# Optimization experiments

Measured on AMD Instinct MI355X. Metric: run time of the kernel, lower is better.

Reference implementation:

```python
import jax, jax.numpy as jnp
import numpy as np

EPS = 1e-5
K = 20


def knn_idx(x, k):
    # x: (B, N, C) -> (B, N, k) indices of k nearest neighbors (incl. self)
    x2 = jnp.sum(x * x, axis=-1)                         # (B, N)
    inner = jnp.einsum('bnc,bmc->bnm', x, x)             # (B, N, N)
    neg_dist = 2.0 * inner - x2[:, :, None] - x2[:, None, :]
    _, idx = jax.lax.top_k(neg_dist, k)                  # (B, N, k)
    return idx


def graph_feature(x, idx):
    # x: (B, N, C), idx: (B, N, k) -> (B, N, k, 2C) = cat([x_j - x_i, x_i])
    nbr = jax.vmap(lambda xb, ib: xb[ib])(x, idx)        # (B, N, k, C)
    xi = jnp.broadcast_to(x[:, :, None, :], nbr.shape)
    return jnp.concatenate([nbr - xi, xi], axis=-1)


def bn_lrelu(x, gamma, beta):
    # eval-mode BatchNorm (running_mean=0, running_var=1) + LeakyReLU(0.2)
    y = x * (gamma / jnp.sqrt(1.0 + EPS)) + beta
    return jnp.where(y >= 0, y, 0.2 * y)


def edge_conv(x, W, gamma, beta, k):
    # x: (B, N, C) -> (B, N, O); 1x1 conv over edge features + max over k
    idx = knn_idx(x, k)
    feat = graph_feature(x, idx)                         # (B, N, k, 2C)
    y = jnp.einsum('bnkc,oc->bnko', feat, W)
    y = bn_lrelu(y, gamma, beta)
    return jnp.max(y, axis=2)                            # (B, N, O)


def setup_inputs() -> dict:
    key = jax.random.key(0)
    ks = jax.random.split(key, 7)
    d = {
        'points': jax.random.normal(ks[0], (8, 2048, 3), dtype=jnp.float32),
        'W1': jax.random.normal(ks[1], (64, 6), dtype=jnp.float32) * 0.1,
        'W2': jax.random.normal(ks[2], (64, 128), dtype=jnp.float32) * 0.1,
        'W3': jax.random.normal(ks[3], (128, 128), dtype=jnp.float32) * 0.1,
        'W4': jax.random.normal(ks[4], (256, 256), dtype=jnp.float32) * 0.1,
        'W5': jax.random.normal(ks[5], (1024, 512), dtype=jnp.float32) * 0.1,
    }
    for name, c in [('1', 64), ('2', 64), ('3', 128), ('4', 256), ('5', 1024)]:
        d['g' + name] = jnp.ones((c,), dtype=jnp.float32)
        d['b' + name] = jnp.zeros((c,), dtype=jnp.float32)
    return d


def reference(points, W1, W2, W3, W4, W5, g1, g2, g3, g4, g5, b1, b2, b3, b4, b5):
    x1 = edge_conv(points, W1, g1, b1, K)                # (B, N, 64)
    x2 = edge_conv(x1, W2, g2, b2, K)                    # (B, N, 64)
    x3 = edge_conv(x2, W3, g3, b3, K)                    # (B, N, 128)
    x4 = edge_conv(x3, W4, g4, b4, K)                    # (B, N, 256)
    x_cat = jnp.concatenate([x1, x2, x3, x4], axis=-1)   # (B, N, 512)
    feat = bn_lrelu(jnp.einsum('bnc,oc->bno', x_cat, W5), g5, b5)  # (B, N, 1024)
    max_pool = jnp.max(feat, axis=1)
    avg_pool = jnp.mean(feat, axis=1)
    return jnp.concatenate([max_pool, avg_pool], axis=-1)  # (B, 2048)
```

## Files before the change

kernel.cpp:

```cpp
#include <hip/hip_runtime.h>
#include <math.h>

#define BATCH 8
#define NPTS 2048
#define KNN 20
#define BN_TOTAL (BATCH * NPTS)
#define EPSV 1e-5f

typedef __attribute__((ext_vector_type(8))) short short8v;
typedef __attribute__((ext_vector_type(4))) float floatx4;

__global__ __launch_bounds__(256) void x2_kernel(const float* __restrict__ x, int C, int ldx,
                                                 float* __restrict__ x2) {
    int i = blockIdx.x * 256 + threadIdx.x;
    if (i >= BN_TOTAL) return;
    const float* xr = x + (size_t)i * ldx;
    float s = 0.f;
    if ((ldx & 3) == 0 && (C & 3) == 0) {
        const float4* xr4 = (const float4*)xr;
        for (int c = 0; c < (C >> 2); ++c) {
            float4 v = xr4[c];
            s = fmaf(v.x, v.x, s); s = fmaf(v.y, v.y, s);
            s = fmaf(v.z, v.z, s); s = fmaf(v.w, v.w, s);
        }
    } else {
        for (int c = 0; c < C; ++c) s = fmaf(xr[c], xr[c], s);
    }
    x2[i] = s;
}

__global__ __launch_bounds__(256) void dist_kernel(const float* __restrict__ x,
                                                   const float* __restrict__ x2,
                                                   int C, int ldx, int b0,
                                                   float* __restrict__ S) {
    __shared__ float As[16][132];
    __shared__ float Bs[16][132];
    int z = blockIdx.z;
    int b = b0 + z;
    int i0 = blockIdx.x * 128, j0 = blockIdx.y * 128;
    const float* xb = x + (size_t)b * NPTS * ldx;
    int tid = threadIdx.x;
    int tm = tid >> 4, tn = tid & 15;

    float acc[8][8] = {};
    int KT = (C + 15) >> 4;
    for (int kt = 0; kt < KT; ++kt) {
        int k0 = kt << 4;
#pragma unroll
        for (int s = tid; s < 512; s += 256) {
            int r = s >> 2, c4 = s & 3;
            int kk = k0 + c4 * 4;
            float va[4], vb[4];
            if (kk + 3 < C && (ldx & 3) == 0) {
                float4 a = *(const float4*)&xb[(size_t)(i0 + r) * ldx + kk];
                float4 bv = *(const float4*)&xb[(size_t)(j0 + r) * ldx + kk];
                va[0] = a.x; va[1] = a.y; va[2] = a.z; va[3] = a.w;
                vb[0] = bv.x; vb[1] = bv.y; vb[2] = bv.z; vb[3] = bv.w;
            } else {
#pragma unroll
                for (int u = 0; u < 4; ++u) {
                    int k = kk + u;
                    va[u] = (k < C) ? xb[(size_t)(i0 + r) * ldx + k] : 0.f;
                    vb[u] = (k < C) ? xb[(size_t)(j0 + r) * ldx + k] : 0.f;
                }
            }
#pragma unroll
            for (int u = 0; u < 4; ++u) {
                As[c4 * 4 + u][r] = va[u];
                Bs[c4 * 4 + u][r] = vb[u];
            }
        }
        __syncthreads();
#pragma unroll
        for (int k = 0; k < 16; ++k) {
            float4 a0 = *(const float4*)&As[k][tm * 8];
            float4 a1 = *(const float4*)&As[k][tm * 8 + 4];
            float4 c0 = *(const float4*)&Bs[k][tn * 8];
            float4 c1 = *(const float4*)&Bs[k][tn * 8 + 4];
            float av[8] = {a0.x, a0.y, a0.z, a0.w, a1.x, a1.y, a1.z, a1.w};
            float bv[8] = {c0.x, c0.y, c0.z, c0.w, c1.x, c1.y, c1.z, c1.w};
#pragma unroll
            for (int mi = 0; mi < 8; ++mi)
#pragma unroll
                for (int ni = 0; ni < 8; ++ni)
                    acc[mi][ni] = fmaf(av[mi], bv[ni], acc[mi][ni]);
        }
        __syncthreads();
    }

    const float* x2b = x2 + (size_t)b * NPTS;
    float xj[8];
#pragma unroll
    for (int u = 0; u < 8; ++u) xj[u] = x2b[j0 + tn * 8 + u];
#pragma unroll
    for (int mi = 0; mi < 8; ++mi) {
        float xi = x2b[i0 + tm * 8 + mi];
        float4 o0, o1;
        o0.x = 2.f * acc[mi][0] - xi - xj[0];
        o0.y = 2.f * acc[mi][1] - xi - xj[1];
        o0.z = 2.f * acc[mi][2] - xi - xj[2];
        o0.w = 2.f * acc[mi][3] - xi - xj[3];
        o1.x = 2.f * acc[mi][4] - xi - xj[4];
        o1.y = 2.f * acc[mi][5] - xi - xj[5];
        o1.z = 2.f * acc[mi][6] - xi - xj[6];
        o1.w = 2.f * acc[mi][7] - xi - xj[7];
        size_t rowp = ((size_t)z * NPTS + i0 + tm * 8 + mi) * NPTS + j0 + tn * 8;
        *(float4*)&S[rowp] = o0;
        *(float4*)&S[rowp + 4] = o1;
    }
}

__global__ __launch_bounds__(256) void topk_kernel(const float* __restrict__ S, int b0,
                                                   int* __restrict__ idx_out) {
    int lane = threadIdx.x & 63, w = threadIdx.x >> 6;
    int row = blockIdx.x * 4 + w;
    const float4* S4 = (const float4*)(S + (size_t)row * NPTS);

    float v[32];
    float lm = -INFINITY; int li = 0;
#pragma unroll
    for (int r4 = 0; r4 < 8; ++r4) {
        float4 f = S4[lane * 8 + r4];
        v[r4 * 4 + 0] = f.x; v[r4 * 4 + 1] = f.y;
        v[r4 * 4 + 2] = f.z; v[r4 * 4 + 3] = f.w;
    }
#pragma unroll
    for (int q = 0; q < 32; ++q)
        if (v[q] > lm) { lm = v[q]; li = q; }

    int sel = 0;
    for (int it = 0; it < KNN; ++it) {
        float bv = lm;
        int bi = (lane << 5) | li;
#pragma unroll
        for (int d = 1; d < 64; d <<= 1) {
            float ov = __shfl_xor(bv, d);
            int oi = __shfl_xor(bi, d);
            if (ov > bv || (ov == bv && oi < bi)) { bv = ov; bi = oi; }
        }
        if (lane == it) sel = bi;
        if ((bi >> 5) == lane) {
            int r = bi & 31;
#pragma unroll
            for (int q = 0; q < 32; ++q)
                if (q == r) v[q] = -INFINITY;
            lm = -INFINITY; li = 0;
#pragma unroll
            for (int q = 0; q < 32; ++q)
                if (v[q] > lm) { lm = v[q]; li = q; }
        }
    }
    int z = row >> 11, i = row & 2047;
    int bn = (b0 + z) * NPTS + i;
    if (lane < KNN) idx_out[bn * KNN + lane] = sel;
}

__global__ __launch_bounds__(256) void pq_gemm(const float* __restrict__ X, int C, int ldx,
                                               const float* __restrict__ W, int O,
                                               float* __restrict__ PQ) {
    __shared__ float As[32][68];
    __shared__ float Bs[32][68];
    int i0 = blockIdx.x * 64, j0 = blockIdx.y * 64;
    int tid = threadIdx.x;
    int tm = tid >> 4, tn = tid & 15;
    int N2 = 2 * O;

    float acc[4][4] = {};
    int KT = (C + 31) >> 5;
    for (int kt = 0; kt < KT; ++kt) {
        int k0 = kt << 5;
        for (int e = tid; e < 2048; e += 256) {
            int m = e >> 5, k = e & 31;
            int kk = k0 + k;
            As[k][m] = (kk < C) ? X[(size_t)(i0 + m) * ldx + kk] : 0.f;
            int o = j0 + m;
            float wv = 0.f;
            if (kk < C)
                wv = (o < O) ? W[(size_t)o * 2 * C + kk] : W[(size_t)(o - O) * 2 * C + C + kk];
            Bs[k][m] = wv;
        }
        __syncthreads();
#pragma unroll
        for (int k = 0; k < 32; ++k) {
            float4 a = *(const float4*)&As[k][tm * 4];
            float4 bb = *(const float4*)&Bs[k][tn * 4];
            float av[4] = {a.x, a.y, a.z, a.w};
            float bv[4] = {bb.x, bb.y, bb.z, bb.w};
#pragma unroll
            for (int mi = 0; mi < 4; ++mi)
#pragma unroll
                for (int ni = 0; ni < 4; ++ni)
                    acc[mi][ni] = fmaf(av[mi], bv[ni], acc[mi][ni]);
        }
        __syncthreads();
    }
#pragma unroll
    for (int mi = 0; mi < 4; ++mi) {
        float4 o;
        o.x = acc[mi][0]; o.y = acc[mi][1]; o.z = acc[mi][2]; o.w = acc[mi][3];
        *(float4*)&PQ[(size_t)(i0 + tm * 4 + mi) * N2 + j0 + tn * 4] = o;
    }
}

__global__ __launch_bounds__(256) void gmax_kernel(const float* __restrict__ PQ,
                                                   const int* __restrict__ idx, int O, int oshift,
                                                   const float* __restrict__ gamma,
                                                   const float* __restrict__ beta,
                                                   float* __restrict__ out, int ldo) {
    __shared__ int s_idx[4][KNN];
    int rpb = 256 >> oshift;
    int lr = threadIdx.x >> oshift;
    int o = threadIdx.x & (O - 1);
    int bn = blockIdx.x * rpb + lr;
    int b = bn >> 11;
    if (o < KNN) s_idx[lr][o] = idx[bn * KNN + o];
    __syncthreads();
    const float inv = 1.0f / sqrtf(1.0f + EPSV);
    int N2 = 2 * O;
    size_t brow = (size_t)(b << 11);
    float mx = -INFINITY, mn = INFINITY;
#pragma unroll
    for (int k = 0; k < KNN; ++k) {
        float v = PQ[(brow + s_idx[lr][k]) * N2 + o];
        mx = fmaxf(mx, v);
        mn = fminf(mn, v);
    }
    float pn = PQ[(size_t)bn * N2 + o];
    float qn = PQ[(size_t)bn * N2 + O + o];
    float sc = gamma[o] * inv;
    float m = (sc >= 0.f) ? mx : mn;
    float z = sc * (m - pn + qn) + beta[o];
    out[(size_t)bn * ldo + o] = (z >= 0.f) ? z : 0.2f * z;
}

__device__ __forceinline__ unsigned short bf16_rne(float x) {
    union { float f; unsigned u; } cv; cv.f = x;
    unsigned r = (cv.u + 0x7fffu + ((cv.u >> 16) & 1u)) >> 16;
    return (unsigned short)r;
}
__global__ __launch_bounds__(256) void split_bf16_kernel(const float* __restrict__ in, int n4,
                                                         unsigned short* __restrict__ hi,
                                                         unsigned short* __restrict__ lo) {
    int i = blockIdx.x * 256 + threadIdx.x;
    if (i >= n4) return;
    float4 v = ((const float4*)in)[i];
    float vv[4] = {v.x, v.y, v.z, v.w};
    ushort4 h, l;
    unsigned short hh[4], ll[4];
#pragma unroll
    for (int u = 0; u < 4; ++u) {
        unsigned short hb = bf16_rne(vv[u]);
        union { unsigned u32; float f; } hf; hf.u32 = ((unsigned)hb) << 16;
        hh[u] = hb;
        ll[u] = bf16_rne(vv[u] - hf.f);
    }
    h.x = hh[0]; h.y = hh[1]; h.z = hh[2]; h.w = hh[3];
    l.x = ll[0]; l.y = ll[1]; l.z = ll[2]; l.w = ll[3];
    *(ushort4*)(hi + (size_t)i * 4) = h;
    *(ushort4*)(lo + (size_t)i * 4) = l;
}

__global__ __launch_bounds__(256) void final_mfma(const unsigned short* __restrict__ Xhi,
                                                  const unsigned short* __restrict__ Xlo,
                                                  const unsigned short* __restrict__ Whi,
                                                  const unsigned short* __restrict__ Wlo,
                                                  const float* __restrict__ g5,
                                                  const float* __restrict__ b5,
                                                  float* __restrict__ part) {
    __shared__ __align__(16) char As[128 * 64];
    __shared__ __align__(16) char Bs[128 * 64];
    __shared__ float sredM[2][128];
    __shared__ float sredS[2][128];

    int tid = threadIdx.x;
    int i0 = blockIdx.x * 128;
    int j0 = blockIdx.y * 128;
    int lane = tid & 63, w = tid >> 6;
    int wr = w >> 1, wc = w & 1;

    int rowA = tid >> 2, q = tid & 3;
    auto swz = [](int row, int qq) { return (row * 64 + qq * 16) ^ ((row & 7) << 4); };
    int wa0 = swz(rowA, q), wa1 = swz(rowA + 64, q);

    int fr = lane & 15, slot = lane >> 4;
    int aoff[4], boff[4];
#pragma unroll
    for (int m = 0; m < 4; ++m) {
        int ra = wr * 64 + m * 16 + fr;
        aoff[m] = (ra * 64 + slot * 16) ^ ((ra & 7) << 4);
        int rb = wc * 64 + m * 16 + fr;
        boff[m] = (rb * 64 + slot * 16) ^ ((rb & 7) << 4);
    }

    floatx4 acc[4][4];
#pragma unroll
    for (int m = 0; m < 4; ++m)
#pragma unroll
        for (int n = 0; n < 4; ++n)
            acc[m][n] = (floatx4){0.f, 0.f, 0.f, 0.f};

    uint4 ra0, ra1, rb0, rb1;
    auto prefetch = [&](int it) {
        int seg = it >> 4;
        int kk = (it & 15) * 32;
        const unsigned short* Ab = ((seg < 2) ? Xhi : Xlo) + (size_t)i0 * 512 + kk + q * 8;
        const unsigned short* Bb = ((seg == 1) ? Wlo : Whi) + (size_t)j0 * 512 + kk + q * 8;
        ra0 = *(const uint4*)(Ab + (size_t)rowA * 512);
        ra1 = *(const uint4*)(Ab + (size_t)(rowA + 64) * 512);
        rb0 = *(const uint4*)(Bb + (size_t)rowA * 512);
        rb1 = *(const uint4*)(Bb + (size_t)(rowA + 64) * 512);
    };

    prefetch(0);
    for (int it = 0; it < 48; ++it) {
        __syncthreads();
        *(uint4*)(As + wa0) = ra0;
        *(uint4*)(As + wa1) = ra1;
        *(uint4*)(Bs + wa0) = rb0;
        *(uint4*)(Bs + wa1) = rb1;
        __syncthreads();
        if (it < 47) prefetch(it + 1);
        short8v af[4], bf[4];
#pragma unroll
        for (int m = 0; m < 4; ++m) af[m] = *(const short8v*)(As + aoff[m]);
#pragma unroll
        for (int n = 0; n < 4; ++n) bf[n] = *(const short8v*)(Bs + boff[n]);
#pragma unroll
        for (int m = 0; m < 4; ++m)
#pragma unroll
            for (int n = 0; n < 4; ++n)
                acc[m][n] = __builtin_amdgcn_mfma_f32_16x16x32_bf16(af[m], bf[n], acc[m][n], 0, 0, 0);
    }

    const float inv = 1.0f / sqrtf(1.0f + EPSV);
#pragma unroll
    for (int n = 0; n < 4; ++n) {
        int o = j0 + wc * 64 + n * 16 + fr;
        float sc = g5[o] * inv;
        float bi = b5[o];
        float mx = -INFINITY, sm = 0.f;
#pragma unroll
        for (int m = 0; m < 4; ++m)
#pragma unroll
            for (int r = 0; r < 4; ++r) {
                float z = fmaf(sc, acc[m][n][r], bi);
                z = (z >= 0.f) ? z : 0.2f * z;
                mx = fmaxf(mx, z);
                sm += z;
            }
#pragma unroll
        for (int d = 16; d < 64; d <<= 1) {
            mx = fmaxf(mx, __shfl_xor(mx, d));
            sm += __shfl_xor(sm, d);
        }
        if (slot == 0) {
            sredM[wr][wc * 64 + n * 16 + fr] = mx;
            sredS[wr][wc * 64 + n * 16 + fr] = sm;
        }
    }
    __syncthreads();
    if (tid < 128) {
        float m = fmaxf(sredM[0][tid], sredM[1][tid]);
        float s = sredS[0][tid] + sredS[1][tid];
        int b = i0 >> 11, nt = (i0 >> 7) & 15;
        size_t base = (size_t)((b * 16 + nt) * 2) * 1024 + j0 + tid;
        part[base] = m;
        part[base + 1024] = s;
    }
}

__global__ __launch_bounds__(256) void freduce_kernel(const float* __restrict__ part,
                                                      float* __restrict__ out) {
    int t = blockIdx.x * 256 + threadIdx.x;
    if (t >= 8 * 1024) return;
    int b = t >> 10, o = t & 1023;
    float m = -INFINITY, s = 0.f;
#pragma unroll
    for (int nt = 0; nt < 16; ++nt) {
        size_t base = (size_t)((b * 16 + nt) * 2) * 1024 + o;
        m = fmaxf(m, part[base]);
        s += part[base + 1024];
    }
    out[b * 2048 + o] = m;
    out[b * 2048 + 1024 + o] = s * (1.0f / 2048.0f);
}

extern "C" void kernel_launch(void* const* d_in, const int* in_sizes, int n_in,
                              void* d_out, int out_size, void* d_ws, size_t ws_size,
                              hipStream_t stream) {
    const float* points = (const float*)d_in[0];
    const float* W1 = (const float*)d_in[1];
    const float* W2 = (const float*)d_in[2];
    const float* W3 = (const float*)d_in[3];
    const float* W4 = (const float*)d_in[4];
    const float* W5 = (const float*)d_in[5];
    const float* g1 = (const float*)d_in[6];
    const float* b1 = (const float*)d_in[7];
    const float* g2 = (const float*)d_in[8];
    const float* b2 = (const float*)d_in[9];
    const float* g3 = (const float*)d_in[10];
    const float* b3 = (const float*)d_in[11];
    const float* g4 = (const float*)d_in[12];
    const float* b4 = (const float*)d_in[13];
    const float* g5 = (const float*)d_in[14];
    const float* b5 = (const float*)d_in[15];
    float* out = (float*)d_out;

    const size_t f_xcat = (size_t)BN_TOTAL * 512;
    const size_t f_w5 = (size_t)1024 * 512;
    const size_t f_x2 = BN_TOTAL;
    const size_t f_idx = (size_t)BN_TOTAL * KNN;
    const size_t f_part = (size_t)8 * 16 * 2 * 1024;
    const size_t f_bf16 = f_xcat + f_w5;
    const size_t fixedf = f_xcat + f_x2 + f_idx + f_part + f_bf16;
    auto needB = [&](int c) {
        size_t spq = (size_t)c * NPTS * NPTS;
        if (spq < f_xcat) spq = f_xcat;
        return 4ull * (fixedf + spq);
    };
    int cB = 2;
    if (ws_size >= needB(8)) cB = 8;
    else if (ws_size >= needB(4)) cB = 4;
    size_t spq_f = (size_t)cB * NPTS * NPTS;
    if (spq_f < f_xcat) spq_f = f_xcat;

    float* xcat = (float*)d_ws;
    float* SPQ = xcat + f_xcat;
    float* x2 = SPQ + spq_f;
    int* idx = (int*)(x2 + f_x2);
    float* part = (float*)(idx + f_idx);
    unsigned short* Xhi = (unsigned short*)(part + f_part);
    unsigned short* Xlo = Xhi + f_xcat;
    unsigned short* Whi = Xlo + f_xcat;
    unsigned short* Wlo = Whi + f_w5;

    auto layer = [&](const float* xin, int C, int ldx, const float* W, int O, int oshift,
                     const float* ga, const float* be, float* xout) {
        x2_kernel<<<(BN_TOTAL + 255) / 256, 256, 0, stream>>>(xin, C, ldx, x2);
        for (int b0 = 0; b0 < BATCH; b0 += cB) {
            dist_kernel<<<dim3(16, 16, cB), 256, 0, stream>>>(xin, x2, C, ldx, b0, SPQ);
            topk_kernel<<<cB * 512, 256, 0, stream>>>(SPQ, b0, idx);
        }
        pq_gemm<<<dim3(BN_TOTAL / 64, (2 * O) / 64), 256, 0, stream>>>(xin, C, ldx, W, O, SPQ);
        int rpb = 256 >> oshift;
        gmax_kernel<<<BN_TOTAL / rpb, 256, 0, stream>>>(SPQ, idx, O, oshift, ga, be, xout, 512);
    };

    layer(points,     3,   3,   W1, 64,  6, g1, b1, xcat + 0);
    layer(xcat + 0,   64,  512, W2, 64,  6, g2, b2, xcat + 64);
    layer(xcat + 64,  64,  512, W3, 128, 7, g3, b3, xcat + 128);
    layer(xcat + 128, 128, 512, W4, 256, 8, g4, b4, xcat + 256);

    split_bf16_kernel<<<(int)((f_xcat / 4 + 255) / 256), 256, 0, stream>>>(xcat, (int)(f_xcat / 4), Xhi, Xlo);
    split_bf16_kernel<<<(int)((f_w5 / 4 + 255) / 256), 256, 0, stream>>>(W5, (int)(f_w5 / 4), Whi, Wlo);
    final_mfma<<<dim3(BN_TOTAL / 128, 1024 / 128), 256, 0, stream>>>(Xhi, Xlo, Whi, Wlo, g5, b5, part);
    freduce_kernel<<<(8 * 1024 + 255) / 256, 256, 0, stream>>>(part, out);
}
```

Baseline: 966.1 us.

## Fuse distance GEMM and top-k selection into one streaming KNN kernel

Replaces the separate distance-matrix kernel (which wrote a full per-batch NxN score matrix to global memory) and the top-k kernel with a single templated kernel. Each block owns 64 query rows, streams over 128-column candidate tiles and keeps a running top-20 list per row in shared memory, using ballot and shuffle reductions to insert only candidates that beat the current minimum. This removes the large global write and read of the score matrix and the batch-chunk launch loop. In exchange the grid is small (256 blocks), insertion work is serialized per row, and the host code specializes launches per layer.

```diff
diff --git a/kernel.cpp b/kernel.cpp
--- a/kernel.cpp
+++ b/kernel.cpp
@@ -29,130 +29,137 @@
     x2[i] = s;
 }
 
-__global__ __launch_bounds__(256) void dist_kernel(const float* __restrict__ x,
-                                                   const float* __restrict__ x2,
-                                                   int C, int ldx, int b0,
-                                                   float* __restrict__ S) {
-    __shared__ float As[16][132];
-    __shared__ float Bs[16][132];
-    int z = blockIdx.z;
-    int b = b0 + z;
-    int i0 = blockIdx.x * 128, j0 = blockIdx.y * 128;
-    const float* xb = x + (size_t)b * NPTS * ldx;
+template <int C, int LDX>
+__global__ __launch_bounds__(512) void knn_fused(const float* __restrict__ x,
+                                                 const float* __restrict__ x2,
+                                                 int* __restrict__ idx_out) {
+    constexpr int BK = (C >= 32) ? 32 : C;
+    constexpr int KT = (C + BK - 1) / BK;
+    __shared__ float As[C][68];
+    __shared__ float Bs[BK][132];
+    __shared__ float tv[64][20];
+    __shared__ int   ti[64][20];
+
     int tid = threadIdx.x;
-    int tm = tid >> 4, tn = tid & 15;
-
-    float acc[8][8] = {};
-    int KT = (C + 15) >> 4;
-    for (int kt = 0; kt < KT; ++kt) {
-        int k0 = kt << 4;
-#pragma unroll
-        for (int s = tid; s < 512; s += 256) {
-            int r = s >> 2, c4 = s & 3;
-            int kk = k0 + c4 * 4;
-            float va[4], vb[4];
-            if (kk + 3 < C && (ldx & 3) == 0) {
-                float4 a = *(const float4*)&xb[(size_t)(i0 + r) * ldx + kk];
-                float4 bv = *(const float4*)&xb[(size_t)(j0 + r) * ldx + kk];
-                va[0] = a.x; va[1] = a.y; va[2] = a.z; va[3] = a.w;
-                vb[0] = bv.x; vb[1] = bv.y; vb[2] = bv.z; vb[3] = bv.w;
+    int b = blockIdx.y;
+    int i0 = blockIdx.x * 64;
+    int bn0 = (b << 11) + i0;
+    const float* xb = x + (size_t)b * NPTS * LDX;
+    const float* x2b = x2 + (b << 11);
+    int tn = tid & 31;
+    int tm = tid >> 5;
+    int g = (tid >> 5) & 1;
+
+    for (int e = tid; e < 64 * KNN; e += 512) {
+        tv[e / KNN][e % KNN] = -INFINITY;
+        ti[e / KNN][e % KNN] = 0x7fffffff;
+    }
+    if (C == 3) {
+        for (int e = tid; e < 64 * 3; e += 512) {
+            int r = e / 3, k = e % 3;
+            As[k][r] = xb[(size_t)(i0 + r) * LDX + k];
+        }
+    } else {
+        for (int e = tid; e < 64 * (C / 4); e += 512) {
+            int r = e / (C / 4), c4 = e % (C / 4);
+            float4 v = *(const float4*)&xb[(size_t)(i0 + r) * LDX + c4 * 4];
+            As[c4 * 4 + 0][r] = v.x; As[c4 * 4 + 1][r] = v.y;
+            As[c4 * 4 + 2][r] = v.z; As[c4 * 4 + 3][r] = v.w;
+        }
+    }
+    float x2i[4];
+#pragma unroll
+    for (int mi = 0; mi < 4; ++mi) x2i[mi] = x2b[i0 + tm * 4 + mi];
+    __syncthreads();
+
+    for (int jt = 0; jt < 16; ++jt) {
+        int j0 = jt << 7;
+        float acc[4][4];
+#pragma unroll
+        for (int mi = 0; mi < 4; ++mi)
+#pragma unroll
+            for (int ni = 0; ni < 4; ++ni) acc[mi][ni] = 0.f;
+
+        for (int kt = 0; kt < KT; ++kt) {
+            __syncthreads();
+            if (C == 3) {
+                for (int e = tid; e < 128 * 3; e += 512) {
+                    int col = e / 3, k = e % 3;
+                    Bs[k][col] = xb[(size_t)(j0 + col) * LDX + k];
+                }
             } else {
-#pragma unroll
-                for (int u = 0; u < 4; ++u) {
-                    int k = kk + u;
-                    va[u] = (k < C) ? xb[(size_t)(i0 + r) * ldx + k] : 0.f;
-                    vb[u] = (k < C) ? xb[(size_t)(j0 + r) * ldx + k] : 0.f;
+                for (int e = tid; e < 128 * (BK / 4); e += 512) {
+                    int col = e >> 3, c4 = e & 7;
+                    float4 v = *(const float4*)&xb[(size_t)(j0 + col) * LDX + kt * BK + c4 * 4];
+                    Bs[c4 * 4 + 0][col] = v.x; Bs[c4 * 4 + 1][col] = v.y;
+                    Bs[c4 * 4 + 2][col] = v.z; Bs[c4 * 4 + 3][col] = v.w;
                 }
             }
-#pragma unroll
-            for (int u = 0; u < 4; ++u) {
-                As[c4 * 4 + u][r] = va[u];
-                Bs[c4 * 4 + u][r] = vb[u];
+            __syncthreads();
+#pragma unroll
+            for (int k = 0; k < BK; ++k) {
+                float4 a = *(const float4*)&As[kt * BK + k][tm * 4];
+                float2 b0 = *(const float2*)&Bs[k][tn * 4];
+                float2 b1 = *(const float2*)&Bs[k][tn * 4 + 2];
+                float av[4] = {a.x, a.y, a.z, a.w};
+                float bv[4] = {b0.x, b0.y, b1.x, b1.y};
+#pragma unroll
+                for (int mi = 0; mi < 4; ++mi)
+#pragma unroll
+                    for (int ni = 0; ni < 4; ++ni)
+                        acc[mi][ni] = fmaf(av[mi], bv[ni], acc[mi][ni]);
             }
         }
-        __syncthreads();
-#pragma unroll
-        for (int k = 0; k < 16; ++k) {
-            float4 a0 = *(const float4*)&As[k][tm * 8];
-            float4 a1 = *(const float4*)&As[k][tm * 8 + 4];
-            float4 c0 = *(const float4*)&Bs[k][tn * 8];
-            float4 c1 = *(const float4*)&Bs[k][tn * 8 + 4];
-            float av[8] = {a0.x, a0.y, a0.z, a0.w, a1.x, a1.y, a1.z, a1.w};
-            float bv[8] = {c0.x, c0.y, c0.z, c0.w, c1.x, c1.y, c1.z, c1.w};
-#pragma unroll
-            for (int mi = 0; mi < 8; ++mi)
-#pragma unroll
-                for (int ni = 0; ni < 8; ++ni)
-                    acc[mi][ni] = fmaf(av[mi], bv[ni], acc[mi][ni]);
-        }
-        __syncthreads();
-    }
-
-    const float* x2b = x2 + (size_t)b * NPTS;
-    float xj[8];
-#pragma unroll
-    for (int u = 0; u < 8; ++u) xj[u] = x2b[j0 + tn * 8 + u];
-#pragma unroll
-    for (int mi = 0; mi < 8; ++mi) {
-        float xi = x2b[i0 + tm * 8 + mi];
-        float4 o0, o1;
-        o0.x = 2.f * acc[mi][0] - xi - xj[0];
-        o0.y = 2.f * acc[mi][1] - xi - xj[1];
-        o0.z = 2.f * acc[mi][2] - xi - xj[2];
-        o0.w = 2.f * acc[mi][3] - xi - xj[3];
-        o1.x = 2.f * acc[mi][4] - xi - xj[4];
-        o1.y = 2.f * acc[mi][5] - xi - xj[5];
-        o1.z = 2.f * acc[mi][6] - xi - xj[6];
-        o1.w = 2.f * acc[mi][7] - xi - xj[7];
-        size_t rowp = ((size_t)z * NPTS + i0 + tm * 8 + mi) * NPTS + j0 + tn * 8;
-        *(float4*)&S[rowp] = o0;
-        *(float4*)&S[rowp + 4] = o1;
-    }
-}
-
-__global__ __launch_bounds__(256) void topk_kernel(const float* __restrict__ S, int b0,
-                                                   int* __restrict__ idx_out) {
-    int lane = threadIdx.x & 63, w = threadIdx.x >> 6;
-    int row = blockIdx.x * 4 + w;
-    const float4* S4 = (const float4*)(S + (size_t)row * NPTS);
-
-    float v[32];
-    float lm = -INFINITY; int li = 0;
-#pragma unroll
-    for (int r4 = 0; r4 < 8; ++r4) {
-        float4 f = S4[lane * 8 + r4];
-        v[r4 * 4 + 0] = f.x; v[r4 * 4 + 1] = f.y;
-        v[r4 * 4 + 2] = f.z; v[r4 * 4 + 3] = f.w;
-    }
-#pragma unroll
-    for (int q = 0; q < 32; ++q)
-        if (v[q] > lm) { lm = v[q]; li = q; }
-
-    int sel = 0;
-    for (int it = 0; it < KNN; ++it) {
-        float bv = lm;
-        int bi = (lane << 5) | li;
-#pragma unroll
-        for (int d = 1; d < 64; d <<= 1) {
-            float ov = __shfl_xor(bv, d);
-            int oi = __shfl_xor(bi, d);
-            if (ov > bv || (ov == bv && oi < bi)) { bv = ov; bi = oi; }
-        }
-        if (lane == it) sel = bi;
-        if ((bi >> 5) == lane) {
-            int r = bi & 31;
-#pragma unroll
-            for (int q = 0; q < 32; ++q)
-                if (q == r) v[q] = -INFINITY;
-            lm = -INFINITY; li = 0;
-#pragma unroll
-            for (int q = 0; q < 32; ++q)
-                if (v[q] > lm) { lm = v[q]; li = q; }
-        }
-    }
-    int z = row >> 11, i = row & 2047;
-    int bn = (b0 + z) * NPTS + i;
-    if (lane < KNN) idx_out[bn * KNN + lane] = sel;
+
+        float x2j[4];
+#pragma unroll
+        for (int u = 0; u < 4; ++u) x2j[u] = x2b[j0 + tn * 4 + u];
+#pragma unroll
+        for (int mi = 0; mi < 4; ++mi)
+#pragma unroll
+            for (int ni = 0; ni < 4; ++ni)
+                acc[mi][ni] = 2.f * acc[mi][ni] - x2i[mi] - x2j[ni];
+
+#pragma unroll
+        for (int mi = 0; mi < 4; ++mi) {
+            int r = tm * 4 + mi;
+            float lmax = acc[mi][0]; int lidx = j0 + tn * 4;
+#pragma unroll
+            for (int ni = 1; ni < 4; ++ni)
+                if (acc[mi][ni] > lmax) { lmax = acc[mi][ni]; lidx = j0 + tn * 4 + ni; }
+            float vmin = tv[r][KNN - 1];
+            unsigned grp = (unsigned)(__ballot(lmax > vmin) >> (g * 32));
+            while (grp) {
+                float bv = lmax; int bj = lidx;
+#pragma unroll
+                for (int d = 1; d < 32; d <<= 1) {
+                    float ov = __shfl_xor(bv, d);
+                    int oj = __shfl_xor(bj, d);
+                    if (ov > bv || (ov == bv && oj < bj)) { bv = ov; bj = oj; }
+                }
+                int p = KNN - 1;
+                while (p > 0 && tv[r][p - 1] < bv) {
+                    tv[r][p] = tv[r][p - 1]; ti[r][p] = ti[r][p - 1]; --p;
+                }
+                tv[r][p] = bv; ti[r][p] = bj;
+                vmin = tv[r][KNN - 1];
+                if (((bj - j0) >> 2) == tn) {
+                    int nk = bj & 3;
+#pragma unroll
+                    for (int ni = 0; ni < 4; ++ni)
+                        if (ni == nk) acc[mi][ni] = -INFINITY;
+                    lmax = acc[mi][0]; lidx = j0 + tn * 4;
+#pragma unroll
+                    for (int ni = 1; ni < 4; ++ni)
+                        if (acc[mi][ni] > lmax) { lmax = acc[mi][ni]; lidx = j0 + tn * 4 + ni; }
+                }
+                grp = (unsigned)(__ballot(lmax > vmin) >> (g * 32));
+            }
+        }
+    }
+    __syncthreads();
+    for (int e = tid; e < 64 * KNN; e += 512)
+        idx_out[(size_t)(bn0 + e / KNN) * KNN + e % KNN] = ti[e / KNN][e % KNN];
 }
 
 __global__ __launch_bounds__(256) void pq_gemm(const float* __restrict__ X, int C, int ldx,
@@ -411,22 +418,10 @@
     const size_t f_x2 = BN_TOTAL;
     const size_t f_idx = (size_t)BN_TOTAL * KNN;
     const size_t f_part = (size_t)8 * 16 * 2 * 1024;
-    const size_t f_bf16 = f_xcat + f_w5;
-    const size_t fixedf = f_xcat + f_x2 + f_idx + f_part + f_bf16;
-    auto needB = [&](int c) {
-        size_t spq = (size_t)c * NPTS * NPTS;
-        if (spq < f_xcat) spq = f_xcat;
-        return 4ull * (fixedf + spq);
-    };
-    int cB = 2;
-    if (ws_size >= needB(8)) cB = 8;
-    else if (ws_size >= needB(4)) cB = 4;
-    size_t spq_f = (size_t)cB * NPTS * NPTS;
-    if (spq_f < f_xcat) spq_f = f_xcat;
 
     float* xcat = (float*)d_ws;
     float* SPQ = xcat + f_xcat;
-    float* x2 = SPQ + spq_f;
+    float* x2 = SPQ + f_xcat;
     int* idx = (int*)(x2 + f_x2);
     float* part = (float*)(idx + f_idx);
     unsigned short* Xhi = (unsigned short*)(part + f_part);
@@ -434,22 +429,25 @@
     unsigned short* Whi = Xlo + f_xcat;
     unsigned short* Wlo = Whi + f_w5;
 
-    auto layer = [&](const float* xin, int C, int ldx, const float* W, int O, int oshift,
-                     const float* ga, const float* be, float* xout) {
-        x2_kernel<<<(BN_TOTAL + 255) / 256, 256, 0, stream>>>(xin, C, ldx, x2);
-        for (int b0 = 0; b0 < BATCH; b0 += cB) {
-            dist_kernel<<<dim3(16, 16, cB), 256, 0, stream>>>(xin, x2, C, ldx, b0, SPQ);
-            topk_kernel<<<cB * 512, 256, 0, stream>>>(SPQ, b0, idx);
-        }
-        pq_gemm<<<dim3(BN_TOTAL / 64, (2 * O) / 64), 256, 0, stream>>>(xin, C, ldx, W, O, SPQ);
-        int rpb = 256 >> oshift;
-        gmax_kernel<<<BN_TOTAL / rpb, 256, 0, stream>>>(SPQ, idx, O, oshift, ga, be, xout, 512);
-    };
-
-    layer(points,     3,   3,   W1, 64,  6, g1, b1, xcat + 0);
-    layer(xcat + 0,   64,  512, W2, 64,  6, g2, b2, xcat + 64);
-    layer(xcat + 64,  64,  512, W3, 128, 7, g3, b3, xcat + 128);
-    layer(xcat + 128, 128, 512, W4, 256, 8, g4, b4, xcat + 256);
+    x2_kernel<<<64, 256, 0, stream>>>(points, 3, 3, x2);
+    knn_fused<3, 3><<<dim3(32, 8), 512, 0, stream>>>(points, x2, idx);
+    pq_gemm<<<dim3(256, 2), 256, 0, stream>>>(points, 3, 3, W1, 64, SPQ);
+    gmax_kernel<<<BN_TOTAL / 4, 256, 0, stream>>>(SPQ, idx, 64, 6, g1, b1, xcat + 0, 512);
+
+    x2_kernel<<<64, 256, 0, stream>>>(xcat + 0, 64, 512, x2);
+    knn_fused<64, 512><<<dim3(32, 8), 512, 0, stream>>>(xcat + 0, x2, idx);
+    pq_gemm<<<dim3(256, 2), 256, 0, stream>>>(xcat + 0, 64, 512, W2, 64, SPQ);
+    gmax_kernel<<<BN_TOTAL / 4, 256, 0, stream>>>(SPQ, idx, 64, 6, g2, b2, xcat + 64, 512);
+
+    x2_kernel<<<64, 256, 0, stream>>>(xcat + 64, 64, 512, x2);
+    knn_fused<64, 512><<<dim3(32, 8), 512, 0, stream>>>(xcat + 64, x2, idx);
+    pq_gemm<<<dim3(256, 4), 256, 0, stream>>>(xcat + 64, 64, 512, W3, 128, SPQ);
+    gmax_kernel<<<BN_TOTAL / 2, 256, 0, stream>>>(SPQ, idx, 128, 7, g3, b3, xcat + 128, 512);
+
+    x2_kernel<<<64, 256, 0, stream>>>(xcat + 128, 128, 512, x2);
+    knn_fused<128, 512><<<dim3(32, 8), 512, 0, stream>>>(xcat + 128, x2, idx);
+    pq_gemm<<<dim3(256, 8), 256, 0, stream>>>(xcat + 128, 128, 512, W4, 256, SPQ);
+    gmax_kernel<<<BN_TOTAL, 256, 0, stream>>>(SPQ, idx, 256, 8, g4, b4, xcat + 256, 512);
 
     split_bf16_kernel<<<(int)((f_xcat / 4 + 255) / 256), 256, 0, stream>>>(xcat, (int)(f_xcat / 4), Xhi, Xlo);
     split_bf16_kernel<<<(int)((f_w5 / 4 + 255) / 256), 256, 0, stream>>>(W5, (int)(f_w5 / 4), Whi, Wlo);
```

Result: slower. 2.547 ms (+163.7%).

## Fuse distance GEMM with per-tile top-k and merge candidates instead of full matrix

Applied to the files above, without the earlier changes.

The distance kernel now runs a local top-20 selection inside each 128x128 tile via 16-lane shuffles and writes only 20 candidates per row per column tile. A second kernel merges the 320 candidates per row into the final 20 neighbours. This removes writing and re-reading the full N×N distance matrix and the batch-chunking loop, and the workspace is restructured into a shared union buffer. The cost is a serial 20-iteration shuffle loop per row inside the GEMM kernel, which adds register pressure and latency.

```diff
diff --git a/kernel.cpp b/kernel.cpp
--- a/kernel.cpp
+++ b/kernel.cpp
@@ -6,6 +6,7 @@
 #define KNN 20
 #define BN_TOTAL (BATCH * NPTS)
 #define EPSV 1e-5f
+#define NT 16
 
 typedef __attribute__((ext_vector_type(8))) short short8v;
 typedef __attribute__((ext_vector_type(4))) float floatx4;
@@ -29,15 +30,15 @@
     x2[i] = s;
 }
 
-__global__ __launch_bounds__(256) void dist_kernel(const float* __restrict__ x,
+__global__ __launch_bounds__(256) void dtop_kernel(const float* __restrict__ x,
                                                    const float* __restrict__ x2,
-                                                   int C, int ldx, int b0,
-                                                   float* __restrict__ S) {
+                                                   int C, int ldx,
+                                                   float2* __restrict__ cand) {
     __shared__ float As[16][132];
     __shared__ float Bs[16][132];
-    int z = blockIdx.z;
-    int b = b0 + z;
-    int i0 = blockIdx.x * 128, j0 = blockIdx.y * 128;
+    int b = blockIdx.z;
+    int jt = blockIdx.y;
+    int i0 = blockIdx.x * 128, j0 = jt * 128;
     const float* xb = x + (size_t)b * NPTS * ldx;
     int tid = threadIdx.x;
     int tm = tid >> 4, tn = tid & 15;
@@ -95,64 +96,87 @@
 #pragma unroll
     for (int mi = 0; mi < 8; ++mi) {
         float xi = x2b[i0 + tm * 8 + mi];
-        float4 o0, o1;
-        o0.x = 2.f * acc[mi][0] - xi - xj[0];
-        o0.y = 2.f * acc[mi][1] - xi - xj[1];
-        o0.z = 2.f * acc[mi][2] - xi - xj[2];
-        o0.w = 2.f * acc[mi][3] - xi - xj[3];
-        o1.x = 2.f * acc[mi][4] - xi - xj[4];
-        o1.y = 2.f * acc[mi][5] - xi - xj[5];
-        o1.z = 2.f * acc[mi][6] - xi - xj[6];
-        o1.w = 2.f * acc[mi][7] - xi - xj[7];
-        size_t rowp = ((size_t)z * NPTS + i0 + tm * 8 + mi) * NPTS + j0 + tn * 8;
-        *(float4*)&S[rowp] = o0;
-        *(float4*)&S[rowp + 4] = o1;
-    }
-}
-
-__global__ __launch_bounds__(256) void topk_kernel(const float* __restrict__ S, int b0,
-                                                   int* __restrict__ idx_out) {
+#pragma unroll
+        for (int ni = 0; ni < 8; ++ni)
+            acc[mi][ni] = 2.f * acc[mi][ni] - xi - xj[ni];
+    }
+
+#pragma unroll
+    for (int mi = 0; mi < 8; ++mi) {
+        float lv = acc[mi][0]; int lu = 0;
+#pragma unroll
+        for (int u = 1; u < 8; ++u)
+            if (acc[mi][u] > lv) { lv = acc[mi][u]; lu = u; }
+        int lj = j0 + tn * 8 + lu;
+        float w0v = -INFINITY, w1v = -INFINITY;
+        int w0j = 0x7fffffff, w1j = 0x7fffffff;
+#pragma unroll 1
+        for (int it = 0; it < KNN; ++it) {
+            float bv = lv; int bj = lj;
+#pragma unroll
+            for (int d = 1; d < 16; d <<= 1) {
+                float ov = __shfl_xor(bv, d);
+                int oj = __shfl_xor(bj, d);
+                if (ov > bv || (ov == bv && oj < bj)) { bv = ov; bj = oj; }
+            }
+            if (it < 16) { if (tn == it) { w0v = bv; w0j = bj; } }
+            else         { if (tn == it - 16) { w1v = bv; w1j = bj; } }
+            if (bj == lj) {
+                int r = lj - j0 - tn * 8;
+#pragma unroll
+                for (int u = 0; u < 8; ++u)
+                    if (u == r) acc[mi][u] = -INFINITY;
+                lv = acc[mi][0]; lu = 0;
+#pragma unroll
+                for (int u = 1; u < 8; ++u)
+                    if (acc[mi][u] > lv) { lv = acc[mi][u]; lu = u; }
+                lj = j0 + tn * 8 + lu;
+            }
+        }
+        float2* cr = cand + ((size_t)(b << 11) + i0 + tm * 8 + mi) * (NT * 20) + jt * 20;
+        cr[tn] = make_float2(w0v, __int_as_float(w0j));
+        if (tn < 4) cr[16 + tn] = make_float2(w1v, __int_as_float(w1j));
+    }
+}
+
+__global__ __launch_bounds__(256) void ktop_merge(const float2* __restrict__ cand,
+                                                  int* __restrict__ idx_out) {
     int lane = threadIdx.x & 63, w = threadIdx.x >> 6;
     int row = blockIdx.x * 4 + w;
-    const float4* S4 = (const float4*)(S + (size_t)row * NPTS);
-
-    float v[32];
-    float lm = -INFINITY; int li = 0;
-#pragma unroll
-    for (int r4 = 0; r4 < 8; ++r4) {
-        float4 f = S4[lane * 8 + r4];
-        v[r4 * 4 + 0] = f.x; v[r4 * 4 + 1] = f.y;
-        v[r4 * 4 + 2] = f.z; v[r4 * 4 + 3] = f.w;
-    }
-#pragma unroll
-    for (int q = 0; q < 32; ++q)
-        if (v[q] > lm) { lm = v[q]; li = q; }
+    const float2* cr = cand + (size_t)row * (NT * 20);
+    float v[5]; int j[5];
+#pragma unroll
+    for (int u = 0; u < 5; ++u) {
+        float2 c = cr[lane + u * 64];
+        v[u] = c.x; j[u] = __float_as_int(c.y);
+    }
+    float lv = v[0]; int lj = j[0];
+#pragma unroll
+    for (int u = 1; u < 5; ++u)
+        if (v[u] > lv || (v[u] == lv && j[u] < lj)) { lv = v[u]; lj = j[u]; }
 
     int sel = 0;
+#pragma unroll 1
     for (int it = 0; it < KNN; ++it) {
-        float bv = lm;
-        int bi = (lane << 5) | li;
+        float bv = lv; int bj = lj;
 #pragma unroll
         for (int d = 1; d < 64; d <<= 1) {
             float ov = __shfl_xor(bv, d);
-            int oi = __shfl_xor(bi, d);
-            if (ov > bv || (ov == bv && oi < bi)) { bv = ov; bi = oi; }
-        }
-        if (lane == it) sel = bi;
-        if ((bi >> 5) == lane) {
-            int r = bi & 31;
-#pragma unroll
-            for (int q = 0; q < 32; ++q)
-                if (q == r) v[q] = -INFINITY;
-            lm = -INFINITY; li = 0;
-#pragma unroll
-            for (int q = 0; q < 32; ++q)
-                if (v[q] > lm) { lm = v[q]; li = q; }
-        }
-    }
-    int z = row >> 11, i = row & 2047;
-    int bn = (b0 + z) * NPTS + i;
-    if (lane < KNN) idx_out[bn * KNN + lane] = sel;
+            int oj = __shfl_xor(bj, d);
+            if (ov > bv || (ov == bv && oj < bj)) { bv = ov; bj = oj; }
+        }
+        if (lane == it) sel = bj;
+        if (bj == lj) {
+#pragma unroll
+            for (int u = 0; u < 5; ++u)
+                if (j[u] == bj) { v[u] = -INFINITY; j[u] = 0x7fffffff; }
+            lv = v[0]; lj = j[0];
+#pragma unroll
+            for (int u = 1; u < 5; ++u)
+                if (v[u] > lv || (v[u] == lv && j[u] < lj)) { lv = v[u]; lj = j[u]; }
+        }
+    }
+    if (lane < KNN) idx_out[(size_t)row * KNN + lane] = sel;
 }
 
 __global__ __launch_bounds__(256) void pq_gemm(const float* __restrict__ X, int C, int ldx,
@@ -408,39 +432,28 @@
 
     const size_t f_xcat = (size_t)BN_TOTAL * 512;
     const size_t f_w5 = (size_t)1024 * 512;
+    const size_t f_union = (size_t)BN_TOTAL * (NT * 20) * 2;
     const size_t f_x2 = BN_TOTAL;
     const size_t f_idx = (size_t)BN_TOTAL * KNN;
     const size_t f_part = (size_t)8 * 16 * 2 * 1024;
-    const size_t f_bf16 = f_xcat + f_w5;
-    const size_t fixedf = f_xcat + f_x2 + f_idx + f_part + f_bf16;
-    auto needB = [&](int c) {
-        size_t spq = (size_t)c * NPTS * NPTS;
-        if (spq < f_xcat) spq = f_xcat;
-        return 4ull * (fixedf + spq);
-    };
-    int cB = 2;
-    if (ws_size >= needB(8)) cB = 8;
-    else if (ws_size >= needB(4)) cB = 4;
-    size_t spq_f = (size_t)cB * NPTS * NPTS;
-    if (spq_f < f_xcat) spq_f = f_xcat;
 
     float* xcat = (float*)d_ws;
-    float* SPQ = xcat + f_xcat;
-    float* x2 = SPQ + spq_f;
-    int* idx = (int*)(x2 + f_x2);
-    float* part = (float*)(idx + f_idx);
-    unsigned short* Xhi = (unsigned short*)(part + f_part);
+    float* U = xcat + f_xcat;
+    float* SPQ = U;
+    float2* cand = (float2*)U;
+    unsigned short* Xhi = (unsigned short*)U;
     unsigned short* Xlo = Xhi + f_xcat;
     unsigned short* Whi = Xlo + f_xcat;
     unsigned short* Wlo = Whi + f_w5;
+    float* x2 = U + f_union;
+    int* idx = (int*)(x2 + f_x2);
+    float* part = (float*)(idx + f_idx);
 
     auto layer = [&](const float* xin, int C, int ldx, const float* W, int O, int oshift,
                      const float* ga, const float* be, float* xout) {
-        x2_kernel<<<(BN_TOTAL + 255) / 256, 256, 0, stream>>>(xin, C, ldx, x2);
-        for (int b0 = 0; b0 < BATCH; b0 += cB) {
-            dist_kernel<<<dim3(16, 16, cB), 256, 0, stream>>>(xin, x2, C, ldx, b0, SPQ);
-            topk_kernel<<<cB * 512, 256, 0, stream>>>(SPQ, b0, idx);
-        }
+        x2_kernel<<<64, 256, 0, stream>>>(xin, C, ldx, x2);
+        dtop_kernel<<<dim3(16, NT, 8), 256, 0, stream>>>(xin, x2, C, ldx, cand);
+        ktop_merge<<<BN_TOTAL / 4, 256, 0, stream>>>(cand, idx);
         pq_gemm<<<dim3(BN_TOTAL / 64, (2 * O) / 64), 256, 0, stream>>>(xin, C, ldx, W, O, SPQ);
         int rpb = 256 >> oshift;
         gmax_kernel<<<BN_TOTAL / rpb, 256, 0, stream>>>(SPQ, idx, O, oshift, ga, be, xout, 512);
```

Result: slower. 1.559 ms (+61.4%).
